# Kernel optimization log

Hardware: AMD Instinct MI355X
Metric: run time of the kernel (lower is better)

Reference implementation:

```python
import jax, jax.numpy as jnp
import numpy as np

NEG_SLOPE = 0.2

def setup_inputs() -> dict:
    key = jax.random.key(0)
    k1, k2, k3, k4 = jax.random.split(key, 4)
    bs, n, f_in, f_out, n_head = 8, 2048, 64, 32, 4
    h = jax.random.normal(k1, (bs, n, f_in), dtype=jnp.float32)
    # xavier_uniform-like scales (exact init values irrelevant for correctness baseline)
    w = jax.random.normal(k2, (n_head, f_in, f_out), dtype=jnp.float32) * 0.14
    a_src = jax.random.normal(k3, (n_head, f_out, 1), dtype=jnp.float32) * 0.3
    a_dst = jax.random.normal(k4, (n_head, f_out, 1), dtype=jnp.float32) * 0.3
    b = jnp.zeros((f_out,), dtype=jnp.float32)
    return {"h": h, "w": w, "a_src": a_src, "a_dst": a_dst, "b": b}

def reference(h, w, a_src, a_dst, b):
    # h: [bs, n, f_in]; w: [H, f_in, f_out]
    h_prime = jnp.einsum('bnf,hfo->bhno', h, w)            # [bs, H, n, f_out]
    attn_src = jnp.einsum('bhno,hot->bhnt', h_prime, a_src)  # [bs, H, n, 1]
    attn_dst = jnp.einsum('bhno,hot->bhnt', h_prime, a_dst)  # [bs, H, n, 1]
    # additive broadcast: score[b,h,i,j] = src[i] + dst[j]
    attn = attn_src + jnp.swapaxes(attn_dst, -1, -2)        # [bs, H, n, n]
    attn = jnp.where(attn >= 0, attn, NEG_SLOPE * attn)     # leaky relu
    attn = jax.nn.softmax(attn, axis=-1)
    # dropout p=0.0 -> identity
    output = jnp.einsum('bhnm,bhmo->bhno', attn, h_prime) + b
    return (output, attn)
```

## Files before the change

kernel.cpp:

```cpp
#include <hip/hip_runtime.h>
#include <hip/hip_bf16.h>

typedef __bf16 bf16x8 __attribute__((ext_vector_type(8)));
typedef float  f32x4  __attribute__((ext_vector_type(4)));

#define LOG2E 1.4426950408889634f

__device__ __forceinline__ float lrelu(float x) { return x >= 0.f ? x : 0.2f * x; }

__device__ __forceinline__ float exp2f_fast(float x) {
#if __has_builtin(__builtin_amdgcn_exp2f)
    return __builtin_amdgcn_exp2f(x);
#else
    return __expf(x * 0.6931471805599453f);
#endif
}

__device__ __forceinline__ unsigned short bfbits(float x) {
    __hip_bfloat16 h = __float2bfloat16(x);
    return *reinterpret_cast<unsigned short*>(&h);
}

__device__ __forceinline__ unsigned packE(float d) {
    const unsigned b1 = bfbits(exp2f_fast(d));
    const unsigned b2 = bfbits(exp2f_fast(0.2f * d));
    return (b1 << 16) | b2;
}

__global__ __launch_bounds__(256) void k_hprime(
    const float* __restrict__ hg,
    const float* __restrict__ wg,
    const float* __restrict__ a_src,
    const float* __restrict__ a_dst,
    __hip_bfloat16* __restrict__ hpF,
    float* __restrict__ srcv,
    float* __restrict__ dstv)
{
    __shared__ float w_lds[64 * 32];
    __shared__ float h_lds[64 * 64];
    __shared__ __hip_bfloat16 t_lds[32 * 72];

    const int t  = threadIdx.x;
    const int bh = blockIdx.x >> 5;
    const int n0 = (blockIdx.x & 31) * 64;
    const int b  = bh >> 2, hh = bh & 3;

    {
        const float4* s4 = (const float4*)(wg + hh * 2048);
        float4* d4 = (float4*)w_lds;
        d4[t] = s4[t];
        d4[t + 256] = s4[t + 256];
        const float4* s4h = (const float4*)(hg + ((size_t)(b * 2048 + n0)) * 64);
        float4* d4h = (float4*)h_lds;
#pragma unroll
        for (int k = 0; k < 4; k++) d4h[t + 256 * k] = s4h[t + 256 * k];
    }
    __syncthreads();

    const int o  = t & 31;
    const int nb = t >> 5;
    float acc[8];
#pragma unroll
    for (int k = 0; k < 8; k++) acc[k] = 0.f;
    for (int f = 0; f < 64; f++) {
        const float wv = w_lds[f * 32 + o];
#pragma unroll
        for (int k = 0; k < 8; k++)
            acc[k] = fmaf(h_lds[(nb + 8 * k) * 64 + f], wv, acc[k]);
    }
    const float as = a_src[hh * 32 + o] * LOG2E;
    const float ad = a_dst[hh * 32 + o] * LOG2E;
#pragma unroll
    for (int k = 0; k < 8; k++) {
        float sv = acc[k] * as;
        float dv = acc[k] * ad;
#pragma unroll
        for (int m = 16; m >= 1; m >>= 1) {
            sv += __shfl_xor(sv, m);
            dv += __shfl_xor(dv, m);
        }
        if (o == 0) {
            const int n = n0 + nb + 8 * k;
            srcv[bh * 2048 + n] = sv;
            dstv[bh * 2048 + n] = dv;
        }
    }
#pragma unroll
    for (int k = 0; k < 8; k++)
        t_lds[o * 72 + nb + 8 * k] = __float2bfloat16(acc[k]);
    __syncthreads();
    {
        const int oo = t >> 3;
        const int ch = t & 7;
        const int jb = ch >> 2, g = ch & 3;
        const __hip_bfloat16* src0 = &t_lds[oo * 72 + jb * 32 + g * 4];
        union { unsigned long long q[2]; uint4 v; } u;
        u.q[0] = *(const unsigned long long*)(src0);
        u.q[1] = *(const unsigned long long*)(src0 + 16);
        *(uint4*)(hpF + ((size_t)(bh * 32 + oo)) * 2048 + n0 + ch * 8) = u.v;
    }
}

__global__ __launch_bounds__(256) void k_main(
    const __hip_bfloat16* __restrict__ hpF,
    const float* __restrict__ srcv,
    const float* __restrict__ dstv,
    const float* __restrict__ bias,
    float* __restrict__ outp,
    float* __restrict__ attn)
{
    __shared__ __attribute__((aligned(16))) float    d_lds[2048];
    __shared__ __attribute__((aligned(16))) unsigned e12[2048];
    __shared__ float ns_lds[64], a1_lds[64], a2_lds[64];
    __shared__ float red[4];

    const int t    = threadIdx.x;
    const int role = blockIdx.x & 1;
    const int wid  = blockIdx.x >> 1;
    const int bh   = wid >> 5;
    const int row0 = (wid & 31) * 64;

    float lmax = -1e30f;
    {
        const float4* s4 = (const float4*)(dstv + bh * 2048);
        float4* d4 = (float4*)d_lds;
#pragma unroll
        for (int k = 0; k < 2; k++) {
            const float4 v = s4[t + 256 * k];
            d4[t + 256 * k] = v;
            lmax = fmaxf(lmax, fmaxf(fmaxf(v.x, v.y), fmaxf(v.z, v.w)));
        }
    }
#pragma unroll
    for (int m = 32; m >= 1; m >>= 1) lmax = fmaxf(lmax, __shfl_xor(lmax, m));
    if ((t & 63) == 0) red[t >> 6] = lmax;
    __syncthreads();
    const float dmax = fmaxf(fmaxf(red[0], red[1]), fmaxf(red[2], red[3]));

    {
#pragma unroll
        for (int k = 0; k < 2; k++) {
            const float4 dv = *((const float4*)d_lds + t + 256 * k);
            uint4 u;
            u.x = packE(dv.x); u.y = packE(dv.y);
            u.z = packE(dv.z); u.w = packE(dv.w);
            *((uint4*)e12 + t + 256 * k) = u;
        }
    }
    __syncthreads();

    {
        const int r = t >> 2, q = t & 3;
        const float s  = srcv[bh * 2048 + row0 + r];
        const float ns = -s;
        float acc1 = 0.f, acc2 = 0.f;
        for (int it = 0; it < 128; it++) {
            const int j = q * 4 + it * 16;
            const float4 dv = *(const float4*)(d_lds + j);
            const uint4  uv = *(const uint4*)(e12 + j);
            { const bool c = dv.x >= ns; acc1 += c ? __uint_as_float(uv.x & 0xffff0000u) : 0.f; acc2 += c ? 0.f : __uint_as_float(uv.x << 16); }
            { const bool c = dv.y >= ns; acc1 += c ? __uint_as_float(uv.y & 0xffff0000u) : 0.f; acc2 += c ? 0.f : __uint_as_float(uv.y << 16); }
            { const bool c = dv.z >= ns; acc1 += c ? __uint_as_float(uv.z & 0xffff0000u) : 0.f; acc2 += c ? 0.f : __uint_as_float(uv.z << 16); }
            { const bool c = dv.w >= ns; acc1 += c ? __uint_as_float(uv.w & 0xffff0000u) : 0.f; acc2 += c ? 0.f : __uint_as_float(uv.w << 16); }
        }
        acc1 += __shfl_xor(acc1, 1); acc1 += __shfl_xor(acc1, 2);
        acc2 += __shfl_xor(acc2, 1); acc2 += __shfl_xor(acc2, 2);
        if (q == 0) {
            const float m  = lrelu(s + dmax);
            const float f1 = exp2f_fast(s - m);
            const float f2 = exp2f_fast(0.2f * s - m);
            const float is = 1.f / (f1 * acc1 + f2 * acc2);
            ns_lds[r] = ns; a1_lds[r] = f1 * is; a2_lds[r] = f2 * is;
        }
    }
    __syncthreads();

    if (role == 0) {
        float* rowbase = attn + ((size_t)(bh * 2048) + row0) * 2048;
        for (int r = 0; r < 64; r++) {
            const float ns = ns_lds[r], a1 = a1_lds[r], a2 = a2_lds[r];
            float* rp = rowbase + (size_t)r * 2048;
#pragma unroll
            for (int h2 = 0; h2 < 2; h2++) {
                const int j = t * 4 + h2 * 1024;
                const float4 dv = *(const float4*)(d_lds + j);
                const uint4  uv = *(const uint4*)(e12 + j);
                f32x4 p;
                { const bool c = dv.x >= ns; p[0] = (c ? a1 : a2) * __uint_as_float(c ? (uv.x & 0xffff0000u) : (uv.x << 16)); }
                { const bool c = dv.y >= ns; p[1] = (c ? a1 : a2) * __uint_as_float(c ? (uv.y & 0xffff0000u) : (uv.y << 16)); }
                { const bool c = dv.z >= ns; p[2] = (c ? a1 : a2) * __uint_as_float(c ? (uv.z & 0xffff0000u) : (uv.z << 16)); }
                { const bool c = dv.w >= ns; p[3] = (c ? a1 : a2) * __uint_as_float(c ? (uv.w & 0xffff0000u) : (uv.w << 16)); }
                *(f32x4*)(rp + j) = p;
            }
        }
    } else {
        const int l  = t & 63, w = t >> 6;
        const int lr = l & 15, g = l >> 4;
        const int rA = w * 16 + lr;
        const float ns = ns_lds[rA], a1 = a1_lds[rA], a2 = a2_lds[rA];
        const __hip_bfloat16* hb0 = hpF + ((size_t)(bh * 32 + lr)) * 2048;
        const __hip_bfloat16* hb1 = hpF + ((size_t)(bh * 32 + 16 + lr)) * 2048;
        f32x4 acc0 = {0.f, 0.f, 0.f, 0.f};
        f32x4 acc1v = {0.f, 0.f, 0.f, 0.f};
        for (int jb = 0; jb < 64; jb++) {
            const int j = jb * 32 + g * 4;
            const float4 dA = *(const float4*)(d_lds + j);
            const float4 dB = *(const float4*)(d_lds + j + 16);
            const uint4  uA = *(const uint4*)(e12 + j);
            const uint4  uB = *(const uint4*)(e12 + j + 16);
            union { unsigned short us[8]; bf16x8 v; } A;
            { const bool c = dA.x >= ns; A.us[0] = bfbits((c ? a1 : a2) * __uint_as_float(c ? (uA.x & 0xffff0000u) : (uA.x << 16))); }
            { const bool c = dA.y >= ns; A.us[1] = bfbits((c ? a1 : a2) * __uint_as_float(c ? (uA.y & 0xffff0000u) : (uA.y << 16))); }
            { const bool c = dA.z >= ns; A.us[2] = bfbits((c ? a1 : a2) * __uint_as_float(c ? (uA.z & 0xffff0000u) : (uA.z << 16))); }
            { const bool c = dA.w >= ns; A.us[3] = bfbits((c ? a1 : a2) * __uint_as_float(c ? (uA.w & 0xffff0000u) : (uA.w << 16))); }
            { const bool c = dB.x >= ns; A.us[4] = bfbits((c ? a1 : a2) * __uint_as_float(c ? (uB.x & 0xffff0000u) : (uB.x << 16))); }
            { const bool c = dB.y >= ns; A.us[5] = bfbits((c ? a1 : a2) * __uint_as_float(c ? (uB.y & 0xffff0000u) : (uB.y << 16))); }
            { const bool c = dB.z >= ns; A.us[6] = bfbits((c ? a1 : a2) * __uint_as_float(c ? (uB.z & 0xffff0000u) : (uB.z << 16))); }
            { const bool c = dB.w >= ns; A.us[7] = bfbits((c ? a1 : a2) * __uint_as_float(c ? (uB.w & 0xffff0000u) : (uB.w << 16))); }
            const bf16x8 b0 = *(const bf16x8*)(hb0 + jb * 32 + g * 8);
            const bf16x8 b1 = *(const bf16x8*)(hb1 + jb * 32 + g * 8);
            acc0  = __builtin_amdgcn_mfma_f32_16x16x32_bf16(A.v, b0, acc0, 0, 0, 0);
            acc1v = __builtin_amdgcn_mfma_f32_16x16x32_bf16(A.v, b1, acc1v, 0, 0, 0);
        }
        const float b0v = bias[lr];
        const float b1v = bias[16 + lr];
#pragma unroll
        for (int reg = 0; reg < 4; reg++) {
            const int grow = row0 + w * 16 + g * 4 + reg;
            float* op = outp + ((size_t)(bh * 2048) + grow) * 32;
            op[lr]      = acc0[reg] + b0v;
            op[16 + lr] = acc1v[reg] + b1v;
        }
    }
}

extern "C" void kernel_launch(void* const* d_in, const int* in_sizes, int n_in,
                              void* d_out, int out_size, void* d_ws, size_t ws_size,
                              hipStream_t stream) {
    (void)in_sizes; (void)n_in; (void)out_size; (void)ws_size;
    const float* h     = (const float*)d_in[0];
    const float* w     = (const float*)d_in[1];
    const float* a_src = (const float*)d_in[2];
    const float* a_dst = (const float*)d_in[3];
    const float* b     = (const float*)d_in[4];

    float* out  = (float*)d_out;
    float* attn = out + (size_t)8 * 4 * 2048 * 32;

    __hip_bfloat16* hpF = (__hip_bfloat16*)d_ws;
    float* srcv = (float*)((char*)d_ws + (size_t)32 * 32 * 2048 * 2);
    float* dstv = srcv + 32 * 2048;

    k_hprime<<<1024, 256, 0, stream>>>(h, w, a_src, a_dst, hpF, srcv, dstv);
    k_main  <<<2048, 256, 0, stream>>>(hpF, srcv, dstv, b, out, attn);
}
```

Before: 161.1 us.

## Split softmax constants into separate kernel and stream attn writes with nontemporal stores

Moves the per-row softmax normalisers and the packed exp table into a new k_consts kernel that writes them to workspace. The fused kernel becomes k_mix: 2048 blocks write attn rows across all 32 batch-heads from a shared exp table using nontemporal stores, and 1024 blocks do the PV MFMA product. The per-element leaky-relu branch is replaced by a branchless fmax of the two scaled exponentials. The goal is to cut redundant per-block setup and improve write bandwidth on the large attn output, at the cost of an extra kernel launch and workspace round-trips.

```diff
diff --git a/kernel.cpp b/kernel.cpp
--- a/kernel.cpp
+++ b/kernel.cpp
@@ -101,33 +101,31 @@
     }
 }
 
-__global__ __launch_bounds__(256) void k_main(
-    const __hip_bfloat16* __restrict__ hpF,
-    const float* __restrict__ srcv,
-    const float* __restrict__ dstv,
-    const float* __restrict__ bias,
-    float* __restrict__ outp,
-    float* __restrict__ attn)
+__global__ __launch_bounds__(256) void k_consts(
+    const float* __restrict__ srcv, const float* __restrict__ dstv,
+    unsigned* __restrict__ e_tab,
+    float* __restrict__ ws_a1, float* __restrict__ ws_a2)
 {
     __shared__ __attribute__((aligned(16))) float    d_lds[2048];
     __shared__ __attribute__((aligned(16))) unsigned e12[2048];
-    __shared__ float ns_lds[64], a1_lds[64], a2_lds[64];
     __shared__ float red[4];
 
     const int t    = threadIdx.x;
-    const int role = blockIdx.x & 1;
-    const int wid  = blockIdx.x >> 1;
+    const int wid  = blockIdx.x;
     const int bh   = wid >> 5;
     const int row0 = (wid & 31) * 64;
 
     float lmax = -1e30f;
     {
         const float4* s4 = (const float4*)(dstv + bh * 2048);
-        float4* d4 = (float4*)d_lds;
 #pragma unroll
         for (int k = 0; k < 2; k++) {
             const float4 v = s4[t + 256 * k];
-            d4[t + 256 * k] = v;
+            *((float4*)d_lds + t + 256 * k) = v;
+            uint4 u;
+            u.x = packE(v.x); u.y = packE(v.y);
+            u.z = packE(v.z); u.w = packE(v.w);
+            *((uint4*)e12 + t + 256 * k) = u;
             lmax = fmaxf(lmax, fmaxf(fmaxf(v.x, v.y), fmaxf(v.z, v.w)));
         }
     }
@@ -137,17 +135,10 @@
     __syncthreads();
     const float dmax = fmaxf(fmaxf(red[0], red[1]), fmaxf(red[2], red[3]));
 
-    {
-#pragma unroll
-        for (int k = 0; k < 2; k++) {
-            const float4 dv = *((const float4*)d_lds + t + 256 * k);
-            uint4 u;
-            u.x = packE(dv.x); u.y = packE(dv.y);
-            u.z = packE(dv.z); u.w = packE(dv.w);
-            *((uint4*)e12 + t + 256 * k) = u;
-        }
-    }
-    __syncthreads();
+    if ((wid & 31) == 0) {
+        *((uint4*)(e_tab + bh * 2048) + t)       = *((const uint4*)e12 + t);
+        *((uint4*)(e_tab + bh * 2048) + t + 256) = *((const uint4*)e12 + t + 256);
+    }
 
     {
         const int r = t >> 2, q = t & 3;
@@ -170,53 +161,92 @@
             const float f1 = exp2f_fast(s - m);
             const float f2 = exp2f_fast(0.2f * s - m);
             const float is = 1.f / (f1 * acc1 + f2 * acc2);
-            ns_lds[r] = ns; a1_lds[r] = f1 * is; a2_lds[r] = f2 * is;
-        }
-    }
-    __syncthreads();
-
-    if (role == 0) {
-        float* rowbase = attn + ((size_t)(bh * 2048) + row0) * 2048;
-        for (int r = 0; r < 64; r++) {
-            const float ns = ns_lds[r], a1 = a1_lds[r], a2 = a2_lds[r];
-            float* rp = rowbase + (size_t)r * 2048;
-#pragma unroll
-            for (int h2 = 0; h2 < 2; h2++) {
-                const int j = t * 4 + h2 * 1024;
-                const float4 dv = *(const float4*)(d_lds + j);
-                const uint4  uv = *(const uint4*)(e12 + j);
+            const int gr = bh * 2048 + row0 + r;
+            ws_a1[gr] = f1 * is; ws_a2[gr] = f2 * is;
+        }
+    }
+}
+
+__global__ __launch_bounds__(256) void k_mix(
+    const __hip_bfloat16* __restrict__ hpF,
+    const unsigned* __restrict__ e_tab,
+    const float* __restrict__ ws_a1, const float* __restrict__ ws_a2,
+    const float* __restrict__ bias,
+    float* __restrict__ outp,
+    float* __restrict__ attn)
+{
+    __shared__ __attribute__((aligned(16))) unsigned e_w[2048];
+    __shared__ __attribute__((aligned(16))) unsigned e_pv[2048];
+    __shared__ float a1_l[64], a2_l[64];
+
+    const int t   = threadIdx.x;
+    const int bid = blockIdx.x;
+    bool is_pv; int rid;
+    if (bid < 2048) { is_pv = (bid & 1) != 0; rid = bid >> 1; }
+    else            { is_pv = false;          rid = 1024 + (bid - 2048); }
+
+    if (!is_pv) {
+        const int wv = t >> 6, l = t & 63;
+        const int g   = rid * 4 + wv;
+        const int row = g >> 2;
+        const int js0 = 2 * (g & 3);
+        float* wbase = attn + (size_t)(2 * g) * 256;
+        for (int i = 0; i < 32; i++) {
+            const uint4 s0 = *((const uint4*)(e_tab + i * 2048) + t);
+            const uint4 s1 = *((const uint4*)(e_tab + i * 2048) + t + 256);
+            const float a1 = ws_a1[i * 2048 + row];
+            const float a2 = ws_a2[i * 2048 + row];
+            __syncthreads();
+            *((uint4*)e_w + t)       = s0;
+            *((uint4*)e_w + t + 256) = s1;
+            __syncthreads();
+            float* chunk = wbase + (size_t)i * (16384 * 256);
+#pragma unroll
+            for (int cc = 0; cc < 2; cc++) {
+                const uint4 uv = *((const uint4*)e_w + (js0 + cc) * 64 + l);
                 f32x4 p;
-                { const bool c = dv.x >= ns; p[0] = (c ? a1 : a2) * __uint_as_float(c ? (uv.x & 0xffff0000u) : (uv.x << 16)); }
-                { const bool c = dv.y >= ns; p[1] = (c ? a1 : a2) * __uint_as_float(c ? (uv.y & 0xffff0000u) : (uv.y << 16)); }
-                { const bool c = dv.z >= ns; p[2] = (c ? a1 : a2) * __uint_as_float(c ? (uv.z & 0xffff0000u) : (uv.z << 16)); }
-                { const bool c = dv.w >= ns; p[3] = (c ? a1 : a2) * __uint_as_float(c ? (uv.w & 0xffff0000u) : (uv.w << 16)); }
-                *(f32x4*)(rp + j) = p;
+                p[0] = fmaxf(a1 * __uint_as_float(uv.x & 0xffff0000u), a2 * __uint_as_float(uv.x << 16));
+                p[1] = fmaxf(a1 * __uint_as_float(uv.y & 0xffff0000u), a2 * __uint_as_float(uv.y << 16));
+                p[2] = fmaxf(a1 * __uint_as_float(uv.z & 0xffff0000u), a2 * __uint_as_float(uv.z << 16));
+                p[3] = fmaxf(a1 * __uint_as_float(uv.w & 0xffff0000u), a2 * __uint_as_float(uv.w << 16));
+                __builtin_nontemporal_store(p, (f32x4*)(chunk + cc * 256 + l * 4));
             }
         }
     } else {
+        const int bh   = rid >> 5;
+        const int row0 = (rid & 31) * 64;
+        {
+            const uint4* s4 = (const uint4*)(e_tab + bh * 2048);
+            *((uint4*)e_pv + t)       = s4[t];
+            *((uint4*)e_pv + t + 256) = s4[t + 256];
+        }
+        if (t < 64) {
+            a1_l[t] = ws_a1[bh * 2048 + row0 + t];
+            a2_l[t] = ws_a2[bh * 2048 + row0 + t];
+        }
+        __syncthreads();
+
         const int l  = t & 63, w = t >> 6;
         const int lr = l & 15, g = l >> 4;
         const int rA = w * 16 + lr;
-        const float ns = ns_lds[rA], a1 = a1_lds[rA], a2 = a2_lds[rA];
+        const float a1 = a1_l[rA], a2 = a2_l[rA];
         const __hip_bfloat16* hb0 = hpF + ((size_t)(bh * 32 + lr)) * 2048;
         const __hip_bfloat16* hb1 = hpF + ((size_t)(bh * 32 + 16 + lr)) * 2048;
-        f32x4 acc0 = {0.f, 0.f, 0.f, 0.f};
+        f32x4 acc0  = {0.f, 0.f, 0.f, 0.f};
         f32x4 acc1v = {0.f, 0.f, 0.f, 0.f};
         for (int jb = 0; jb < 64; jb++) {
             const int j = jb * 32 + g * 4;
-            const float4 dA = *(const float4*)(d_lds + j);
-            const float4 dB = *(const float4*)(d_lds + j + 16);
-            const uint4  uA = *(const uint4*)(e12 + j);
-            const uint4  uB = *(const uint4*)(e12 + j + 16);
+            const uint4 uA = *(const uint4*)(e_pv + j);
+            const uint4 uB = *(const uint4*)(e_pv + j + 16);
             union { unsigned short us[8]; bf16x8 v; } A;
-            { const bool c = dA.x >= ns; A.us[0] = bfbits((c ? a1 : a2) * __uint_as_float(c ? (uA.x & 0xffff0000u) : (uA.x << 16))); }
-            { const bool c = dA.y >= ns; A.us[1] = bfbits((c ? a1 : a2) * __uint_as_float(c ? (uA.y & 0xffff0000u) : (uA.y << 16))); }
-            { const bool c = dA.z >= ns; A.us[2] = bfbits((c ? a1 : a2) * __uint_as_float(c ? (uA.z & 0xffff0000u) : (uA.z << 16))); }
-            { const bool c = dA.w >= ns; A.us[3] = bfbits((c ? a1 : a2) * __uint_as_float(c ? (uA.w & 0xffff0000u) : (uA.w << 16))); }
-            { const bool c = dB.x >= ns; A.us[4] = bfbits((c ? a1 : a2) * __uint_as_float(c ? (uB.x & 0xffff0000u) : (uB.x << 16))); }
-            { const bool c = dB.y >= ns; A.us[5] = bfbits((c ? a1 : a2) * __uint_as_float(c ? (uB.y & 0xffff0000u) : (uB.y << 16))); }
-            { const bool c = dB.z >= ns; A.us[6] = bfbits((c ? a1 : a2) * __uint_as_float(c ? (uB.z & 0xffff0000u) : (uB.z << 16))); }
-            { const bool c = dB.w >= ns; A.us[7] = bfbits((c ? a1 : a2) * __uint_as_float(c ? (uB.w & 0xffff0000u) : (uB.w << 16))); }
+            A.us[0] = bfbits(fmaxf(a1 * __uint_as_float(uA.x & 0xffff0000u), a2 * __uint_as_float(uA.x << 16)));
+            A.us[1] = bfbits(fmaxf(a1 * __uint_as_float(uA.y & 0xffff0000u), a2 * __uint_as_float(uA.y << 16)));
+            A.us[2] = bfbits(fmaxf(a1 * __uint_as_float(uA.z & 0xffff0000u), a2 * __uint_as_float(uA.z << 16)));
+            A.us[3] = bfbits(fmaxf(a1 * __uint_as_float(uA.w & 0xffff0000u), a2 * __uint_as_float(uA.w << 16)));
+            A.us[4] = bfbits(fmaxf(a1 * __uint_as_float(uB.x & 0xffff0000u), a2 * __uint_as_float(uB.x << 16)));
+            A.us[5] = bfbits(fmaxf(a1 * __uint_as_float(uB.y & 0xffff0000u), a2 * __uint_as_float(uB.y << 16)));
+            A.us[6] = bfbits(fmaxf(a1 * __uint_as_float(uB.z & 0xffff0000u), a2 * __uint_as_float(uB.z << 16)));
+            A.us[7] = bfbits(fmaxf(a1 * __uint_as_float(uB.w & 0xffff0000u), a2 * __uint_as_float(uB.w << 16)));
             const bf16x8 b0 = *(const bf16x8*)(hb0 + jb * 32 + g * 8);
             const bf16x8 b1 = *(const bf16x8*)(hb1 + jb * 32 + g * 8);
             acc0  = __builtin_amdgcn_mfma_f32_16x16x32_bf16(A.v, b0, acc0, 0, 0, 0);
@@ -228,7 +258,7 @@
         for (int reg = 0; reg < 4; reg++) {
             const int grow = row0 + w * 16 + g * 4 + reg;
             float* op = outp + ((size_t)(bh * 2048) + grow) * 32;
-            op[lr]      = acc0[reg] + b0v;
+            op[lr]      = acc0[reg]  + b0v;
             op[16 + lr] = acc1v[reg] + b1v;
         }
     }
@@ -247,10 +277,15 @@
     float* out  = (float*)d_out;
     float* attn = out + (size_t)8 * 4 * 2048 * 32;
 
-    __hip_bfloat16* hpF = (__hip_bfloat16*)d_ws;
-    float* srcv = (float*)((char*)d_ws + (size_t)32 * 32 * 2048 * 2);
-    float* dstv = srcv + 32 * 2048;
+    char* wsb = (char*)d_ws;
+    __hip_bfloat16* hpF = (__hip_bfloat16*)wsb;
+    float*    srcv  = (float*)(wsb + (4u << 20));
+    float*    dstv  = srcv + 32 * 2048;
+    float*    ws_a1 = dstv + 32 * 2048;
+    float*    ws_a2 = ws_a1 + 32 * 2048;
+    unsigned* e_tab = (unsigned*)(ws_a2 + 32 * 2048);
 
     k_hprime<<<1024, 256, 0, stream>>>(h, w, a_src, a_dst, hpF, srcv, dstv);
-    k_main  <<<2048, 256, 0, stream>>>(hpF, srcv, dstv, b, out, attn);
-}
+    k_consts<<<1024, 256, 0, stream>>>(srcv, dstv, e_tab, ws_a1, ws_a2);
+    k_mix   <<<3072, 256, 0, stream>>>(hpF, e_tab, ws_a1, ws_a2, b, out, attn);
+}
```

Measured after the change: 188.6 us. 17.1% more time.
